# Performance work log

Hardware: AMD Instinct MI355X
Metric: run time of the kernel (lower is better)

Reference implementation:

```python
import jax, jax.numpy as jnp
import numpy as np

N_NODES = 100000
N_EDGES = 1600000
D_IN, D_H, D_OUT = 256, 128, 128


def setup_inputs() -> dict:
    key = jax.random.key(0)
    ks = jax.random.split(key, 8)
    x = jax.random.normal(ks[0], (N_NODES, D_IN), dtype=jnp.float32)
    edge_index = jax.random.randint(ks[1], (2, N_EDGES), 0, N_NODES, dtype=jnp.int64)
    def glorot(k, fan_in, fan_out):
        s = jnp.sqrt(6.0 / (fan_in + fan_out))
        return jax.random.uniform(k, (fan_in, fan_out), jnp.float32, -s, s)
    W1 = glorot(ks[2], D_IN, D_H)
    b1 = jnp.zeros((D_H,), jnp.float32)
    W2 = glorot(ks[3], D_H, D_H)
    b2 = jnp.zeros((D_H,), jnp.float32)
    W3 = glorot(ks[4], D_H, D_OUT)
    b3 = jnp.zeros((D_OUT,), jnp.float32)
    return {"x": x, "edge_index": edge_index,
            "W1": W1, "b1": b1, "W2": W2, "b2": b2, "W3": W3, "b3": b3}


def _gcn_norm(edge_index, n_nodes):
    # PyG GCNConv: add self-loops, symmetric normalization D^-1/2 (A+I) D^-1/2
    loop = jnp.arange(n_nodes, dtype=edge_index.dtype)
    src = jnp.concatenate([edge_index[0], loop])  # source j
    dst = jnp.concatenate([edge_index[1], loop])  # target i
    deg = jax.ops.segment_sum(jnp.ones_like(dst, dtype=jnp.float32), dst,
                              num_segments=n_nodes)
    dinv = jnp.where(deg > 0, jax.lax.rsqrt(deg), 0.0)
    norm = dinv[src] * dinv[dst]  # [E+N]
    return src, dst, norm


def _gcn_conv(h, W, b, src, dst, norm, n_nodes):
    h = h @ W                                   # [N, d_out] transform first
    msg = h[src] * norm[:, None]                # gather + edge-weight
    out = jax.ops.segment_sum(msg, dst, num_segments=n_nodes)  # scatter-add
    return out + b


def reference(x, edge_index, W1, b1, W2, b2, W3, b3):
    n = x.shape[0]
    src, dst, norm = _gcn_norm(edge_index, n)
    h = jax.nn.relu(_gcn_conv(x, W1, b1, src, dst, norm, n))
    h = jax.nn.relu(_gcn_conv(h, W2, b2, src, dst, norm, n))
    return _gcn_conv(h, W3, b3, src, dst, norm, n)
```

## Files before the change

### kernel.cpp

```cpp
#include <hip/hip_runtime.h>
#include <hip/hip_fp16.h>
#include <math.h>


#define N_NODES 100000
#define N_EDGES 1600000

typedef _Float16 f16x8 __attribute__((ext_vector_type(8)));
typedef float    f32x4 __attribute__((ext_vector_type(4)));


__global__ __launch_bounds__(256) void k_zero_int(int* __restrict__ p, int n) {
    int i = blockIdx.x * 256 + threadIdx.x;
    if (i < n) p[i] = 0;
}

__global__ __launch_bounds__(256) void k_count(const int* __restrict__ dst, int* __restrict__ cnt, int E) {
    int e = blockIdx.x * 256 + threadIdx.x;
    if (e < E) atomicAdd(&cnt[dst[e]], 1);
}

__global__ __launch_bounds__(256) void k_scan_block(const int* __restrict__ cnt, int* __restrict__ excl,
                                                    int* __restrict__ bsum, int n) {
    __shared__ int s[256];
    int i = blockIdx.x * 256 + threadIdx.x;
    int v = (i < n) ? ((cnt[i] + 7) & ~7) : 0;
    s[threadIdx.x] = v;
    __syncthreads();
    #pragma unroll
    for (int off = 1; off < 256; off <<= 1) {
        int t = (threadIdx.x >= (unsigned)off) ? s[threadIdx.x - off] : 0;
        __syncthreads();
        s[threadIdx.x] += t;
        __syncthreads();
    }
    if (i < n) excl[i] = s[threadIdx.x] - v;
    if (threadIdx.x == 255) bsum[blockIdx.x] = s[255];
}

__global__ __launch_bounds__(512) void k_scan_partials(int* __restrict__ bsum, int nb) {
    __shared__ int s[512];
    int tid = threadIdx.x;
    int v = (tid < nb) ? bsum[tid] : 0;
    s[tid] = v;
    __syncthreads();
    #pragma unroll
    for (int off = 1; off < 512; off <<= 1) {
        int t = (tid >= (unsigned)off) ? s[tid - off] : 0;
        __syncthreads();
        s[tid] += t;
        __syncthreads();
    }
    if (tid < nb) bsum[tid] = s[tid] - v;
}

__global__ __launch_bounds__(256) void k_finalize(const int* __restrict__ excl, const int* __restrict__ bsum,
                                                  const int* __restrict__ cnt, int* __restrict__ rowptr,
                                                  int* __restrict__ fill, float* __restrict__ dinv, int n) {
    int i = blockIdx.x * 256 + threadIdx.x;
    if (i < n) {
        int rp = excl[i] + bsum[i >> 8];
        rowptr[i] = rp;
        fill[i]   = rp;
        dinv[i]   = rsqrtf((float)(cnt[i] + 1));
    }
}

__global__ __launch_bounds__(256) void k_init_csr(int* __restrict__ csr, int n, unsigned int* __restrict__ phz) {
    int i = blockIdx.x * 256 + threadIdx.x;
    if (i < n) csr[i] = N_NODES;
    if (blockIdx.x == 0 && threadIdx.x < 64) phz[threadIdx.x] = 0;
}

__global__ __launch_bounds__(256) void k_fill_edges(const int* __restrict__ src, const int* __restrict__ dst,
                                                    int* __restrict__ fill, int* __restrict__ csr,
                                                    int E, int lo, int hi) {
    int e = blockIdx.x * 256 + threadIdx.x;
    if (e < E) {
        int d = dst[e];
        if (d >= lo && d < hi) {
            int p = atomicAdd(&fill[d], 1);
            csr[p] = src[e];
        }
    }
}

__global__ __launch_bounds__(256) void k_wpack(const float* __restrict__ W, _Float16* __restrict__ Wpk, int K) {
    int j = blockIdx.x * 256 + threadIdx.x;
    if (j < K * 128) {
        int i  = j & 7;
        int l  = (j >> 3) & 63;
        int tc = (j >> 9) & 7;
        int c  = j >> 12;
        int col = tc * 16 + (l & 15);
        int k   = c * 32 + (l >> 4) * 8 + i;
        float w = W[(size_t)k * 128 + col];
        _Float16 h = (_Float16)w;
        Wpk[j] = h;
        Wpk[(size_t)K * 128 + j] = (_Float16)(w - (float)h);
    }
}


template <int K>
__global__ __launch_bounds__(256) void k_gemm_mfma(const float* __restrict__ X,
                                                   const _Float16* __restrict__ Wpk,
                                                   const float* __restrict__ dinv,
                                                   _Float16* __restrict__ Y, int n) {
    constexpr int NC = K / 32;
    __shared__ float sX[64 * 32];
    const int t    = threadIdx.x;
    const int wave = t >> 6;
    const int lane = t & 63;
    const int lrow = lane & 15;
    const int kgrp = lane >> 4;
    const int row0 = blockIdx.x * 64;
    const int R    = wave * 16 + lrow;
    const _Float16* __restrict__ Wlo = Wpk + (size_t)K * 128;

    const int rs0 = t >> 3,        gs = t & 7;
    const int rs1 = (t >> 3) + 32;
    const int gc0 = (gs ^ (rs0 & 7)) << 2;
    const int gc1 = (gs ^ (rs1 & 7)) << 2;
    const int gr0 = row0 + rs0, gr1 = row0 + rs1;
    const bool ok0 = gr0 < n, ok1 = gr1 < n;
    const float* __restrict__ xr0 = X + (size_t)gr0 * K;
    const float* __restrict__ xr1 = X + (size_t)gr1 * K;

    f32x4 acc[8];
    #pragma unroll
    for (int i = 0; i < 8; ++i) acc[i] = (f32x4){0.f, 0.f, 0.f, 0.f};

    const float4 z4 = make_float4(0.f, 0.f, 0.f, 0.f);
    float4 rv0 = ok0 ? *(const float4*)&xr0[gc0] : z4;
    float4 rv1 = ok1 ? *(const float4*)&xr1[gc1] : z4;
    *(float4*)&sX[(rs0 * 8 + gs) * 4] = rv0;
    *(float4*)&sX[(rs1 * 8 + gs) * 4] = rv1;
    __syncthreads();

    #pragma unroll
    for (int c = 0; c < NC; ++c) {
        if (c + 1 < NC) {
            rv0 = ok0 ? *(const float4*)&xr0[(c + 1) * 32 + gc0] : z4;
            rv1 = ok1 ? *(const float4*)&xr1[(c + 1) * 32 + gc1] : z4;
        }
        float4 x0 = *(const float4*)&sX[(R * 8 + ((kgrp * 2)     ^ (R & 7))) * 4];
        float4 x1 = *(const float4*)&sX[(R * 8 + ((kgrp * 2 + 1) ^ (R & 7))) * 4];
        float xs[8] = {x0.x, x0.y, x0.z, x0.w, x1.x, x1.y, x1.z, x1.w};
        f16x8 ah, al;
        #pragma unroll
        for (int i = 0; i < 8; ++i) {
            _Float16 h = (_Float16)xs[i];
            ah[i] = h;
            al[i] = (_Float16)(xs[i] - (float)h);
        }
        const size_t wb = ((size_t)(c * 8) * 64 + lane) * 8;
        #pragma unroll
        for (int tc = 0; tc < 8; ++tc) {
            f16x8 bh = *(const f16x8*)(Wpk + wb + (size_t)tc * 512);
            f16x8 bl = *(const f16x8*)(Wlo + wb + (size_t)tc * 512);
            acc[tc] = __builtin_amdgcn_mfma_f32_16x16x32_f16(ah, bh, acc[tc], 0, 0, 0);
            acc[tc] = __builtin_amdgcn_mfma_f32_16x16x32_f16(al, bh, acc[tc], 0, 0, 0);
            acc[tc] = __builtin_amdgcn_mfma_f32_16x16x32_f16(ah, bl, acc[tc], 0, 0, 0);
        }
        if (c + 1 < NC) {
            __syncthreads();
            *(float4*)&sX[(rs0 * 8 + gs) * 4] = rv0;
            *(float4*)&sX[(rs1 * 8 + gs) * 4] = rv1;
            __syncthreads();
        }
    }

    #pragma unroll
    for (int r = 0; r < 4; ++r) {
        int grow = row0 + wave * 16 + kgrp * 4 + r;
        if (grow < n) {
            float dv = dinv[grow];
            _Float16* yr = Y + (size_t)grow * 128 + lrow;
            #pragma unroll
            for (int tc = 0; tc < 8; ++tc) yr[tc * 16] = (_Float16)(dv * acc[tc][r]);
        }
    }
}


__device__ __forceinline__ void acc8(float a[8], uint4 u) {
    float2 p;
    p = __half22float2(*(__half2*)&u.x); a[0] += p.x; a[1] += p.y;
    p = __half22float2(*(__half2*)&u.y); a[2] += p.x; a[3] += p.y;
    p = __half22float2(*(__half2*)&u.z); a[4] += p.x; a[5] += p.y;
    p = __half22float2(*(__half2*)&u.w); a[6] += p.x; a[7] += p.y;
}

template <bool RELU>
__global__ __launch_bounds__(256) void k_agg(const __half* __restrict__ H, const int* __restrict__ rowptr,
                                             const int* __restrict__ cnt, const int* __restrict__ csr,
                                             const float* __restrict__ dinv, const float* __restrict__ bias,
                                             float* __restrict__ out, int n) {
    const int lane  = threadIdx.x & 63;
    const int q     = lane >> 4;
    const int fl    = lane & 15;
    const int wave0 = (int)((blockIdx.x * 256 + threadIdx.x) >> 6);
    const int nwave = (int)((gridDim.x * 256) >> 6);
    const uint4* __restrict__ Hu = (const uint4*)H;
    const float4 b0 = *(const float4*)&bias[fl * 8];
    const float4 b1 = *(const float4*)&bias[fl * 8 + 4];

    const int nquad = n >> 2;
    for (int g = wave0; g < nquad; g += nwave) {
        const int node = g * 4 + q;
        float a[8];
        {
            uint4 u = Hu[(size_t)node * 16 + fl];
            float2 p;
            p = __half22float2(*(__half2*)&u.x); a[0] = p.x; a[1] = p.y;
            p = __half22float2(*(__half2*)&u.y); a[2] = p.x; a[3] = p.y;
            p = __half22float2(*(__half2*)&u.z); a[4] = p.x; a[5] = p.y;
            p = __half22float2(*(__half2*)&u.w); a[6] = p.x; a[7] = p.y;
        }

        const int c0 = rowptr[node];
        const int cn = cnt[node];
        for (int e8 = 0; e8 < cn; e8 += 8) {
            const int4* qp = (const int4*)(csr + c0 + e8);
            int4 qa = qp[0], qb = qp[1];
            uint4 u0 = Hu[(size_t)qa.x * 16 + fl];
            uint4 u1 = Hu[(size_t)qa.y * 16 + fl];
            uint4 u2 = Hu[(size_t)qa.z * 16 + fl];
            uint4 u3 = Hu[(size_t)qa.w * 16 + fl];
            uint4 u4 = Hu[(size_t)qb.x * 16 + fl];
            uint4 u5 = Hu[(size_t)qb.y * 16 + fl];
            uint4 u6 = Hu[(size_t)qb.z * 16 + fl];
            uint4 u7 = Hu[(size_t)qb.w * 16 + fl];
            acc8(a, u0); acc8(a, u1); acc8(a, u2); acc8(a, u3);
            acc8(a, u4); acc8(a, u5); acc8(a, u6); acc8(a, u7);
        }

        const float dv = dinv[node];
        float4 o0, o1;
        o0.x = fmaf(dv, a[0], b0.x); o0.y = fmaf(dv, a[1], b0.y);
        o0.z = fmaf(dv, a[2], b0.z); o0.w = fmaf(dv, a[3], b0.w);
        o1.x = fmaf(dv, a[4], b1.x); o1.y = fmaf(dv, a[5], b1.y);
        o1.z = fmaf(dv, a[6], b1.z); o1.w = fmaf(dv, a[7], b1.w);
        if (RELU) {
            o0.x = fmaxf(o0.x, 0.f); o0.y = fmaxf(o0.y, 0.f);
            o0.z = fmaxf(o0.z, 0.f); o0.w = fmaxf(o0.w, 0.f);
            o1.x = fmaxf(o1.x, 0.f); o1.y = fmaxf(o1.y, 0.f);
            o1.z = fmaxf(o1.z, 0.f); o1.w = fmaxf(o1.w, 0.f);
        }
        *(float4*)&out[(size_t)node * 128 + fl * 8]     = o0;
        *(float4*)&out[(size_t)node * 128 + fl * 8 + 4] = o1;
    }
}


extern "C" void kernel_launch(void* const* d_in, const int* in_sizes, int n_in,
                              void* d_out, int out_size, void* d_ws, size_t ws_size,
                              hipStream_t stream) {
    const float* x  = (const float*)d_in[0];
    const int*   ei = (const int*)d_in[1];
    const float* W1 = (const float*)d_in[2];
    const float* b1 = (const float*)d_in[3];
    const float* W2 = (const float*)d_in[4];
    const float* b2 = (const float*)d_in[5];
    const float* W3 = (const float*)d_in[6];
    const float* b3 = (const float*)d_in[7];
    float* out = (float*)d_out;

    const int N = N_NODES, E = N_EDGES;
    const int EP = E + 7 * N + 64;
    const int* src = ei;
    const int* dst = ei + E;

    char* w = (char*)d_ws;
    auto alloc = [&](size_t bytes) -> void* {
        void* p = (void*)w;
        w += (bytes + 255) & ~(size_t)255;
        return p;
    };
    int*      cnt    = (int*)alloc((size_t)N * 4);
    int*      excl   = (int*)alloc((size_t)N * 4);
    int*      bsum   = (int*)alloc(4096);
    int*      rowptr = (int*)alloc((size_t)N * 4);
    int*      fill   = (int*)alloc((size_t)N * 4);
    float*    dinv   = (float*)alloc((size_t)N * 4);
    int*      csr    = (int*)alloc((size_t)EP * 4);
    _Float16* Ph     = (_Float16*)alloc((size_t)(N + 8) * 128 * 2);
    _Float16* Wpk    = (_Float16*)alloc((size_t)2 * 256 * 128 * 2);
    float*    Q      = out;

    const int nbN = (N + 255) / 256;
    const int nbE = (E + 255) / 256;
    const int nbP = (EP + 255) / 256;

    k_zero_int<<<nbN, 256, 0, stream>>>(cnt, N);
    k_count<<<nbE, 256, 0, stream>>>(dst, cnt, E);
    k_scan_block<<<nbN, 256, 0, stream>>>(cnt, excl, bsum, N);
    k_scan_partials<<<1, 512, 0, stream>>>(bsum, nbN);
    k_finalize<<<nbN, 256, 0, stream>>>(excl, bsum, cnt, rowptr, fill, dinv, N);
    k_init_csr<<<nbP, 256, 0, stream>>>(csr, EP, (unsigned int*)(Ph + (size_t)N * 128));
    for (int r = 0; r < 4; ++r) {
        int lo = r * (N / 4);
        int hi = (r == 3) ? N : (r + 1) * (N / 4);
        k_fill_edges<<<nbE, 256, 0, stream>>>(src, dst, fill, csr, E, lo, hi);
    }

    const int gemm_grid = (N + 63) / 64;
    const int agg_grid  = 2048;

    k_wpack<<<(256 * 128 + 255) / 256, 256, 0, stream>>>(W1, Wpk, 256);
    k_gemm_mfma<256><<<gemm_grid, 256, 0, stream>>>(x, Wpk, dinv, Ph, N);
    k_agg<true><<<agg_grid, 256, 0, stream>>>((const __half*)Ph, rowptr, cnt, csr, dinv, b1, Q, N);
    k_wpack<<<(128 * 128 + 255) / 256, 256, 0, stream>>>(W2, Wpk, 128);
    k_gemm_mfma<128><<<gemm_grid, 256, 0, stream>>>(Q, Wpk, dinv, Ph, N);
    k_agg<true><<<agg_grid, 256, 0, stream>>>((const __half*)Ph, rowptr, cnt, csr, dinv, b2, Q, N);
    k_wpack<<<(128 * 128 + 255) / 256, 256, 0, stream>>>(W3, Wpk, 128);
    k_gemm_mfma<128><<<gemm_grid, 256, 0, stream>>>(Q, Wpk, dinv, Ph, N);
    k_agg<false><<<agg_grid, 256, 0, stream>>>((const __half*)Ph, rowptr, cnt, csr, dinv, b3, out, N);
}
```

Baseline: 464.3 us.

## Double GEMM row tile per block and split each node's edges across wave quarters

The MFMA GEMM now handles 128 rows per block: each wave computes two 16-row tiles, so every W fragment load is reused twice, at the cost of more accumulator registers. The aggregation kernel now gives each node a whole wave instead of a 16-lane quarter. The four quarters each gather two neighbours per 8-edge chunk and are combined with cross-lane shuffles. This is meant to even out load imbalance from varying degrees and shorten the per-node dependency chain, but it adds shuffle work and leaves three quarters of the lanes idle during the output write.

```diff
diff --git a/kernel.cpp b/kernel.cpp
--- a/kernel.cpp
+++ b/kernel.cpp
@@ -108,34 +108,48 @@
                                                    const float* __restrict__ dinv,
                                                    _Float16* __restrict__ Y, int n) {
     constexpr int NC = K / 32;
-    __shared__ float sX[64 * 32];
+    __shared__ float sX[128 * 32];
     const int t    = threadIdx.x;
     const int wave = t >> 6;
     const int lane = t & 63;
     const int lrow = lane & 15;
     const int kgrp = lane >> 4;
-    const int row0 = blockIdx.x * 64;
-    const int R    = wave * 16 + lrow;
+    const int row0 = blockIdx.x * 128;
+    const int R0   = wave * 32 + lrow;
+    const int R1   = R0 + 16;
     const _Float16* __restrict__ Wlo = Wpk + (size_t)K * 128;
 
-    const int rs0 = t >> 3,        gs = t & 7;
-    const int rs1 = (t >> 3) + 32;
-    const int gc0 = (gs ^ (rs0 & 7)) << 2;
-    const int gc1 = (gs ^ (rs1 & 7)) << 2;
-    const int gr0 = row0 + rs0, gr1 = row0 + rs1;
-    const bool ok0 = gr0 < n, ok1 = gr1 < n;
-    const float* __restrict__ xr0 = X + (size_t)gr0 * K;
-    const float* __restrict__ xr1 = X + (size_t)gr1 * K;
-
-    f32x4 acc[8];
-    #pragma unroll
-    for (int i = 0; i < 8; ++i) acc[i] = (f32x4){0.f, 0.f, 0.f, 0.f};
+    const int gs  = t & 7;
+    const int rsb = t >> 3;
+    const float* __restrict__ xr0 = X + (size_t)(row0 + rsb)      * K;
+    const float* __restrict__ xr1 = X + (size_t)(row0 + rsb + 32) * K;
+    const float* __restrict__ xr2 = X + (size_t)(row0 + rsb + 64) * K;
+    const float* __restrict__ xr3 = X + (size_t)(row0 + rsb + 96) * K;
+    const bool ok0 = row0 + rsb      < n;
+    const bool ok1 = row0 + rsb + 32 < n;
+    const bool ok2 = row0 + rsb + 64 < n;
+    const bool ok3 = row0 + rsb + 96 < n;
+    const int gc0 = (gs ^ ( rsb       & 7)) << 2;
+    const int gc1 = (gs ^ ((rsb + 32) & 7)) << 2;
+    const int gc2 = (gs ^ ((rsb + 64) & 7)) << 2;
+    const int gc3 = (gs ^ ((rsb + 96) & 7)) << 2;
+
+    f32x4 acc0[8], acc1[8];
+    #pragma unroll
+    for (int i = 0; i < 8; ++i) {
+        acc0[i] = (f32x4){0.f, 0.f, 0.f, 0.f};
+        acc1[i] = (f32x4){0.f, 0.f, 0.f, 0.f};
+    }
 
     const float4 z4 = make_float4(0.f, 0.f, 0.f, 0.f);
     float4 rv0 = ok0 ? *(const float4*)&xr0[gc0] : z4;
     float4 rv1 = ok1 ? *(const float4*)&xr1[gc1] : z4;
-    *(float4*)&sX[(rs0 * 8 + gs) * 4] = rv0;
-    *(float4*)&sX[(rs1 * 8 + gs) * 4] = rv1;
+    float4 rv2 = ok2 ? *(const float4*)&xr2[gc2] : z4;
+    float4 rv3 = ok3 ? *(const float4*)&xr3[gc3] : z4;
+    *(float4*)&sX[((rsb     ) * 8 + gs) * 4] = rv0;
+    *(float4*)&sX[((rsb + 32) * 8 + gs) * 4] = rv1;
+    *(float4*)&sX[((rsb + 64) * 8 + gs) * 4] = rv2;
+    *(float4*)&sX[((rsb + 96) * 8 + gs) * 4] = rv3;
     __syncthreads();
 
     #pragma unroll
@@ -143,42 +157,65 @@
         if (c + 1 < NC) {
             rv0 = ok0 ? *(const float4*)&xr0[(c + 1) * 32 + gc0] : z4;
             rv1 = ok1 ? *(const float4*)&xr1[(c + 1) * 32 + gc1] : z4;
-        }
-        float4 x0 = *(const float4*)&sX[(R * 8 + ((kgrp * 2)     ^ (R & 7))) * 4];
-        float4 x1 = *(const float4*)&sX[(R * 8 + ((kgrp * 2 + 1) ^ (R & 7))) * 4];
-        float xs[8] = {x0.x, x0.y, x0.z, x0.w, x1.x, x1.y, x1.z, x1.w};
-        f16x8 ah, al;
+            rv2 = ok2 ? *(const float4*)&xr2[(c + 1) * 32 + gc2] : z4;
+            rv3 = ok3 ? *(const float4*)&xr3[(c + 1) * 32 + gc3] : z4;
+        }
+        float4 x0a = *(const float4*)&sX[(R0 * 8 + ((kgrp * 2)     ^ (R0 & 7))) * 4];
+        float4 x0b = *(const float4*)&sX[(R0 * 8 + ((kgrp * 2 + 1) ^ (R0 & 7))) * 4];
+        float4 x1a = *(const float4*)&sX[(R1 * 8 + ((kgrp * 2)     ^ (R1 & 7))) * 4];
+        float4 x1b = *(const float4*)&sX[(R1 * 8 + ((kgrp * 2 + 1) ^ (R1 & 7))) * 4];
+        float xs0[8] = {x0a.x, x0a.y, x0a.z, x0a.w, x0b.x, x0b.y, x0b.z, x0b.w};
+        float xs1[8] = {x1a.x, x1a.y, x1a.z, x1a.w, x1b.x, x1b.y, x1b.z, x1b.w};
+        f16x8 ah0, al0, ah1, al1;
         #pragma unroll
         for (int i = 0; i < 8; ++i) {
-            _Float16 h = (_Float16)xs[i];
-            ah[i] = h;
-            al[i] = (_Float16)(xs[i] - (float)h);
+            _Float16 h0 = (_Float16)xs0[i];
+            ah0[i] = h0;
+            al0[i] = (_Float16)(xs0[i] - (float)h0);
+            _Float16 h1 = (_Float16)xs1[i];
+            ah1[i] = h1;
+            al1[i] = (_Float16)(xs1[i] - (float)h1);
         }
         const size_t wb = ((size_t)(c * 8) * 64 + lane) * 8;
         #pragma unroll
         for (int tc = 0; tc < 8; ++tc) {
             f16x8 bh = *(const f16x8*)(Wpk + wb + (size_t)tc * 512);
             f16x8 bl = *(const f16x8*)(Wlo + wb + (size_t)tc * 512);
-            acc[tc] = __builtin_amdgcn_mfma_f32_16x16x32_f16(ah, bh, acc[tc], 0, 0, 0);
-            acc[tc] = __builtin_amdgcn_mfma_f32_16x16x32_f16(al, bh, acc[tc], 0, 0, 0);
-            acc[tc] = __builtin_amdgcn_mfma_f32_16x16x32_f16(ah, bl, acc[tc], 0, 0, 0);
+            acc0[tc] = __builtin_amdgcn_mfma_f32_16x16x32_f16(ah0, bh, acc0[tc], 0, 0, 0);
+            acc0[tc] = __builtin_amdgcn_mfma_f32_16x16x32_f16(al0, bh, acc0[tc], 0, 0, 0);
+            acc0[tc] = __builtin_amdgcn_mfma_f32_16x16x32_f16(ah0, bl, acc0[tc], 0, 0, 0);
+            acc1[tc] = __builtin_amdgcn_mfma_f32_16x16x32_f16(ah1, bh, acc1[tc], 0, 0, 0);
+            acc1[tc] = __builtin_amdgcn_mfma_f32_16x16x32_f16(al1, bh, acc1[tc], 0, 0, 0);
+            acc1[tc] = __builtin_amdgcn_mfma_f32_16x16x32_f16(ah1, bl, acc1[tc], 0, 0, 0);
         }
         if (c + 1 < NC) {
             __syncthreads();
-            *(float4*)&sX[(rs0 * 8 + gs) * 4] = rv0;
-            *(float4*)&sX[(rs1 * 8 + gs) * 4] = rv1;
+            *(float4*)&sX[((rsb     ) * 8 + gs) * 4] = rv0;
+            *(float4*)&sX[((rsb + 32) * 8 + gs) * 4] = rv1;
+            *(float4*)&sX[((rsb + 64) * 8 + gs) * 4] = rv2;
+            *(float4*)&sX[((rsb + 96) * 8 + gs) * 4] = rv3;
             __syncthreads();
         }
     }
 
     #pragma unroll
     for (int r = 0; r < 4; ++r) {
-        int grow = row0 + wave * 16 + kgrp * 4 + r;
+        int grow = row0 + wave * 32 + kgrp * 4 + r;
         if (grow < n) {
             float dv = dinv[grow];
             _Float16* yr = Y + (size_t)grow * 128 + lrow;
             #pragma unroll
-            for (int tc = 0; tc < 8; ++tc) yr[tc * 16] = (_Float16)(dv * acc[tc][r]);
+            for (int tc = 0; tc < 8; ++tc) yr[tc * 16] = (_Float16)(dv * acc0[tc][r]);
+        }
+    }
+    #pragma unroll
+    for (int r = 0; r < 4; ++r) {
+        int grow = row0 + wave * 32 + 16 + kgrp * 4 + r;
+        if (grow < n) {
+            float dv = dinv[grow];
+            _Float16* yr = Y + (size_t)grow * 128 + lrow;
+            #pragma unroll
+            for (int tc = 0; tc < 8; ++tc) yr[tc * 16] = (_Float16)(dv * acc1[tc][r]);
         }
     }
 }
@@ -203,14 +240,10 @@
     const int wave0 = (int)((blockIdx.x * 256 + threadIdx.x) >> 6);
     const int nwave = (int)((gridDim.x * 256) >> 6);
     const uint4* __restrict__ Hu = (const uint4*)H;
-    const float4 b0 = *(const float4*)&bias[fl * 8];
-    const float4 b1 = *(const float4*)&bias[fl * 8 + 4];
-
-    const int nquad = n >> 2;
-    for (int g = wave0; g < nquad; g += nwave) {
-        const int node = g * 4 + q;
-        float a[8];
-        {
+
+    for (int node = wave0; node < n; node += nwave) {
+        float a[8] = {0.f, 0.f, 0.f, 0.f, 0.f, 0.f, 0.f, 0.f};
+        if (q == 0) {
             uint4 u = Hu[(size_t)node * 16 + fl];
             float2 p;
             p = __half22float2(*(__half2*)&u.x); a[0] = p.x; a[1] = p.y;
@@ -221,35 +254,39 @@
 
         const int c0 = rowptr[node];
         const int cn = cnt[node];
-        for (int e8 = 0; e8 < cn; e8 += 8) {
-            const int4* qp = (const int4*)(csr + c0 + e8);
-            int4 qa = qp[0], qb = qp[1];
-            uint4 u0 = Hu[(size_t)qa.x * 16 + fl];
-            uint4 u1 = Hu[(size_t)qa.y * 16 + fl];
-            uint4 u2 = Hu[(size_t)qa.z * 16 + fl];
-            uint4 u3 = Hu[(size_t)qa.w * 16 + fl];
-            uint4 u4 = Hu[(size_t)qb.x * 16 + fl];
-            uint4 u5 = Hu[(size_t)qb.y * 16 + fl];
-            uint4 u6 = Hu[(size_t)qb.z * 16 + fl];
-            uint4 u7 = Hu[(size_t)qb.w * 16 + fl];
-            acc8(a, u0); acc8(a, u1); acc8(a, u2); acc8(a, u3);
-            acc8(a, u4); acc8(a, u5); acc8(a, u6); acc8(a, u7);
-        }
-
-        const float dv = dinv[node];
-        float4 o0, o1;
-        o0.x = fmaf(dv, a[0], b0.x); o0.y = fmaf(dv, a[1], b0.y);
-        o0.z = fmaf(dv, a[2], b0.z); o0.w = fmaf(dv, a[3], b0.w);
-        o1.x = fmaf(dv, a[4], b1.x); o1.y = fmaf(dv, a[5], b1.y);
-        o1.z = fmaf(dv, a[6], b1.z); o1.w = fmaf(dv, a[7], b1.w);
-        if (RELU) {
-            o0.x = fmaxf(o0.x, 0.f); o0.y = fmaxf(o0.y, 0.f);
-            o0.z = fmaxf(o0.z, 0.f); o0.w = fmaxf(o0.w, 0.f);
-            o1.x = fmaxf(o1.x, 0.f); o1.y = fmaxf(o1.y, 0.f);
-            o1.z = fmaxf(o1.z, 0.f); o1.w = fmaxf(o1.w, 0.f);
-        }
-        *(float4*)&out[(size_t)node * 128 + fl * 8]     = o0;
-        *(float4*)&out[(size_t)node * 128 + fl * 8 + 4] = o1;
+        #pragma unroll 2
+        for (int e = 0; e < cn; e += 8) {
+            int2 id = *(const int2*)&csr[c0 + e + 2 * q];
+            uint4 u0 = Hu[(size_t)id.x * 16 + fl];
+            uint4 u1 = Hu[(size_t)id.y * 16 + fl];
+            acc8(a, u0);
+            acc8(a, u1);
+        }
+
+        #pragma unroll
+        for (int i = 0; i < 8; ++i) {
+            a[i] += __shfl_xor(a[i], 16);
+            a[i] += __shfl_xor(a[i], 32);
+        }
+
+        if (q == 0) {
+            const float dv = dinv[node];
+            const float4 b0 = *(const float4*)&bias[fl * 8];
+            const float4 b1 = *(const float4*)&bias[fl * 8 + 4];
+            float4 o0, o1;
+            o0.x = fmaf(dv, a[0], b0.x); o0.y = fmaf(dv, a[1], b0.y);
+            o0.z = fmaf(dv, a[2], b0.z); o0.w = fmaf(dv, a[3], b0.w);
+            o1.x = fmaf(dv, a[4], b1.x); o1.y = fmaf(dv, a[5], b1.y);
+            o1.z = fmaf(dv, a[6], b1.z); o1.w = fmaf(dv, a[7], b1.w);
+            if (RELU) {
+                o0.x = fmaxf(o0.x, 0.f); o0.y = fmaxf(o0.y, 0.f);
+                o0.z = fmaxf(o0.z, 0.f); o0.w = fmaxf(o0.w, 0.f);
+                o1.x = fmaxf(o1.x, 0.f); o1.y = fmaxf(o1.y, 0.f);
+                o1.z = fmaxf(o1.z, 0.f); o1.w = fmaxf(o1.w, 0.f);
+            }
+            *(float4*)&out[(size_t)node * 128 + fl * 8]     = o0;
+            *(float4*)&out[(size_t)node * 128 + fl * 8 + 4] = o1;
+        }
     }
 }
 
@@ -305,7 +342,7 @@
         k_fill_edges<<<nbE, 256, 0, stream>>>(src, dst, fill, csr, E, lo, hi);
     }
 
-    const int gemm_grid = (N + 63) / 64;
+    const int gemm_grid = (N + 127) / 128;
     const int agg_grid  = 2048;
 
     k_wpack<<<(256 * 128 + 255) / 256, 256, 0, stream>>>(W1, Wpk, 256);
```

Result: slower. 478.4 us (+3.0%).

## Hold W fragments in registers and split output columns across waves in MFMA GEMM

Applied to the files above, without the earlier changes.

Each wave now owns 32 output columns across all 64 rows and loads its W hi/lo fragments into registers once, instead of re-reading W from global memory for every K chunk. X is converted to the fp16 hi/lo split once per element during staging and stored in double-buffered shared memory, so the conversion is no longer repeated by every wave, and one barrier per chunk is removed. The cost is many more registers for preloaded W (NC*4 f16x8 vectors), which for K=256 may lower occupancy.

```diff
diff --git a/kernel.cpp b/kernel.cpp
--- a/kernel.cpp
+++ b/kernel.cpp
@@ -108,77 +108,100 @@
                                                    const float* __restrict__ dinv,
                                                    _Float16* __restrict__ Y, int n) {
     constexpr int NC = K / 32;
-    __shared__ float sX[64 * 32];
+    __shared__ __align__(16) _Float16 sAh[2][4][64][8];
+    __shared__ __align__(16) _Float16 sAl[2][4][64][8];
     const int t    = threadIdx.x;
     const int wave = t >> 6;
     const int lane = t & 63;
     const int lrow = lane & 15;
     const int kgrp = lane >> 4;
     const int row0 = blockIdx.x * 64;
-    const int R    = wave * 16 + lrow;
     const _Float16* __restrict__ Wlo = Wpk + (size_t)K * 128;
 
-    const int rs0 = t >> 3,        gs = t & 7;
-    const int rs1 = (t >> 3) + 32;
-    const int gc0 = (gs ^ (rs0 & 7)) << 2;
-    const int gc1 = (gs ^ (rs1 & 7)) << 2;
-    const int gr0 = row0 + rs0, gr1 = row0 + rs1;
-    const bool ok0 = gr0 < n, ok1 = gr1 < n;
-    const float* __restrict__ xr0 = X + (size_t)gr0 * K;
-    const float* __restrict__ xr1 = X + (size_t)gr1 * K;
-
-    f32x4 acc[8];
-    #pragma unroll
-    for (int i = 0; i < 8; ++i) acc[i] = (f32x4){0.f, 0.f, 0.f, 0.f};
+    f16x8 bh[NC][2], bl[NC][2];
+    #pragma unroll
+    for (int c = 0; c < NC; ++c)
+        #pragma unroll
+        for (int j = 0; j < 2; ++j) {
+            const size_t idx = ((size_t)(c * 8 + wave * 2 + j) * 64 + lane) * 8;
+            bh[c][j] = *(const f16x8*)(Wpk + idx);
+            bl[c][j] = *(const f16x8*)(Wlo + idx);
+        }
+
+    const int srow = t >> 2;
+    const int skg  = t & 3;
+    const int sfrag = srow >> 4;
+    const int slane = (skg << 4) | (srow & 15);
+    const bool sok = row0 + srow < n;
+    const float* __restrict__ xrow = X + (size_t)(row0 + srow) * K + skg * 8;
+
+    f32x4 acc[4][2];
+    #pragma unroll
+    for (int f = 0; f < 4; ++f)
+        #pragma unroll
+        for (int j = 0; j < 2; ++j) acc[f][j] = (f32x4){0.f, 0.f, 0.f, 0.f};
 
     const float4 z4 = make_float4(0.f, 0.f, 0.f, 0.f);
-    float4 rv0 = ok0 ? *(const float4*)&xr0[gc0] : z4;
-    float4 rv1 = ok1 ? *(const float4*)&xr1[gc1] : z4;
-    *(float4*)&sX[(rs0 * 8 + gs) * 4] = rv0;
-    *(float4*)&sX[(rs1 * 8 + gs) * 4] = rv1;
-    __syncthreads();
-
-    #pragma unroll
-    for (int c = 0; c < NC; ++c) {
-        if (c + 1 < NC) {
-            rv0 = ok0 ? *(const float4*)&xr0[(c + 1) * 32 + gc0] : z4;
-            rv1 = ok1 ? *(const float4*)&xr1[(c + 1) * 32 + gc1] : z4;
-        }
-        float4 x0 = *(const float4*)&sX[(R * 8 + ((kgrp * 2)     ^ (R & 7))) * 4];
-        float4 x1 = *(const float4*)&sX[(R * 8 + ((kgrp * 2 + 1) ^ (R & 7))) * 4];
-        float xs[8] = {x0.x, x0.y, x0.z, x0.w, x1.x, x1.y, x1.z, x1.w};
-        f16x8 ah, al;
+    float4 ra = sok ? *(const float4*)&xrow[0] : z4;
+    float4 rb = sok ? *(const float4*)&xrow[4] : z4;
+    {
+        float xs[8] = {ra.x, ra.y, ra.z, ra.w, rb.x, rb.y, rb.z, rb.w};
+        f16x8 hi, lo;
         #pragma unroll
         for (int i = 0; i < 8; ++i) {
             _Float16 h = (_Float16)xs[i];
-            ah[i] = h;
-            al[i] = (_Float16)(xs[i] - (float)h);
-        }
-        const size_t wb = ((size_t)(c * 8) * 64 + lane) * 8;
-        #pragma unroll
-        for (int tc = 0; tc < 8; ++tc) {
-            f16x8 bh = *(const f16x8*)(Wpk + wb + (size_t)tc * 512);
-            f16x8 bl = *(const f16x8*)(Wlo + wb + (size_t)tc * 512);
-            acc[tc] = __builtin_amdgcn_mfma_f32_16x16x32_f16(ah, bh, acc[tc], 0, 0, 0);
-            acc[tc] = __builtin_amdgcn_mfma_f32_16x16x32_f16(al, bh, acc[tc], 0, 0, 0);
-            acc[tc] = __builtin_amdgcn_mfma_f32_16x16x32_f16(ah, bl, acc[tc], 0, 0, 0);
-        }
+            hi[i] = h;
+            lo[i] = (_Float16)(xs[i] - (float)h);
+        }
+        *(f16x8*)&sAh[0][sfrag][slane][0] = hi;
+        *(f16x8*)&sAl[0][sfrag][slane][0] = lo;
+    }
+    __syncthreads();
+
+    #pragma unroll
+    for (int c = 0; c < NC; ++c) {
+        const int cur = c & 1;
         if (c + 1 < NC) {
+            ra = sok ? *(const float4*)&xrow[(c + 1) * 32] : z4;
+            rb = sok ? *(const float4*)&xrow[(c + 1) * 32 + 4] : z4;
+        }
+        #pragma unroll
+        for (int f = 0; f < 4; ++f) {
+            f16x8 ah = *(const f16x8*)&sAh[cur][f][lane][0];
+            f16x8 al = *(const f16x8*)&sAl[cur][f][lane][0];
+            #pragma unroll
+            for (int j = 0; j < 2; ++j) {
+                acc[f][j] = __builtin_amdgcn_mfma_f32_16x16x32_f16(ah, bh[c][j], acc[f][j], 0, 0, 0);
+                acc[f][j] = __builtin_amdgcn_mfma_f32_16x16x32_f16(al, bh[c][j], acc[f][j], 0, 0, 0);
+                acc[f][j] = __builtin_amdgcn_mfma_f32_16x16x32_f16(ah, bl[c][j], acc[f][j], 0, 0, 0);
+            }
+        }
+        if (c + 1 < NC) {
+            float xs[8] = {ra.x, ra.y, ra.z, ra.w, rb.x, rb.y, rb.z, rb.w};
+            f16x8 hi, lo;
+            #pragma unroll
+            for (int i = 0; i < 8; ++i) {
+                _Float16 h = (_Float16)xs[i];
+                hi[i] = h;
+                lo[i] = (_Float16)(xs[i] - (float)h);
+            }
+            *(f16x8*)&sAh[cur ^ 1][sfrag][slane][0] = hi;
+            *(f16x8*)&sAl[cur ^ 1][sfrag][slane][0] = lo;
             __syncthreads();
-            *(float4*)&sX[(rs0 * 8 + gs) * 4] = rv0;
-            *(float4*)&sX[(rs1 * 8 + gs) * 4] = rv1;
-            __syncthreads();
-        }
-    }
-
-    #pragma unroll
-    for (int r = 0; r < 4; ++r) {
-        int grow = row0 + wave * 16 + kgrp * 4 + r;
-        if (grow < n) {
-            float dv = dinv[grow];
-            _Float16* yr = Y + (size_t)grow * 128 + lrow;
-            #pragma unroll
-            for (int tc = 0; tc < 8; ++tc) yr[tc * 16] = (_Float16)(dv * acc[tc][r]);
+        }
+    }
+
+    #pragma unroll
+    for (int f = 0; f < 4; ++f) {
+        #pragma unroll
+        for (int r = 0; r < 4; ++r) {
+            int grow = row0 + f * 16 + kgrp * 4 + r;
+            if (grow < n) {
+                float dv = dinv[grow];
+                _Float16* yr = Y + (size_t)grow * 128 + wave * 32 + lrow;
+                yr[0]  = (_Float16)(dv * acc[f][0][r]);
+                yr[16] = (_Float16)(dv * acc[f][1][r]);
+            }
         }
     }
 }
```

After: 533.8 us. +15.0%, slower.

## Stage 128-wide K slabs in padded LDS for GEMM; split degree count into four node ranges

Applied to the files above, without the earlier changes.

The GEMM now loads 128 columns of X per stage into a padded LDS tile (stride 33 float4) instead of 32 columns per stage with an XOR swizzle. This cuts the number of barrier/refill rounds to one or two per block, at the cost of more LDS per block, which may lower occupancy. The degree-count kernel is also split into four launches, each handling only destination nodes in one quarter of the node range. This narrows the atomic footprint per pass, the same approach the existing fill_edges step already uses, but it reads the edge list four times.

```diff
diff --git a/kernel.cpp b/kernel.cpp
--- a/kernel.cpp
+++ b/kernel.cpp
@@ -15,9 +15,13 @@
     if (i < n) p[i] = 0;
 }
 
-__global__ __launch_bounds__(256) void k_count(const int* __restrict__ dst, int* __restrict__ cnt, int E) {
+__global__ __launch_bounds__(256) void k_count(const int* __restrict__ dst, int* __restrict__ cnt,
+                                               int E, int lo, int hi) {
     int e = blockIdx.x * 256 + threadIdx.x;
-    if (e < E) atomicAdd(&cnt[dst[e]], 1);
+    if (e < E) {
+        int d = dst[e];
+        if (d >= lo && d < hi) atomicAdd(&cnt[d], 1);
+    }
 }
 
 __global__ __launch_bounds__(256) void k_scan_block(const int* __restrict__ cnt, int* __restrict__ excl,
@@ -107,8 +111,8 @@
                                                    const _Float16* __restrict__ Wpk,
                                                    const float* __restrict__ dinv,
                                                    _Float16* __restrict__ Y, int n) {
-    constexpr int NC = K / 32;
-    __shared__ float sX[64 * 32];
+    constexpr int NS = K / 128;
+    __shared__ float sX[64 * 33 * 4];
     const int t    = threadIdx.x;
     const int wave = t >> 6;
     const int lane = t & 63;
@@ -118,55 +122,63 @@
     const int R    = wave * 16 + lrow;
     const _Float16* __restrict__ Wlo = Wpk + (size_t)K * 128;
 
-    const int rs0 = t >> 3,        gs = t & 7;
-    const int rs1 = (t >> 3) + 32;
-    const int gc0 = (gs ^ (rs0 & 7)) << 2;
-    const int gc1 = (gs ^ (rs1 & 7)) << 2;
-    const int gr0 = row0 + rs0, gr1 = row0 + rs1;
-    const bool ok0 = gr0 < n, ok1 = gr1 < n;
-    const float* __restrict__ xr0 = X + (size_t)gr0 * K;
-    const float* __restrict__ xr1 = X + (size_t)gr1 * K;
+    const int sr = t >> 5;
+    const int sg = t & 31;
 
     f32x4 acc[8];
     #pragma unroll
     for (int i = 0; i < 8; ++i) acc[i] = (f32x4){0.f, 0.f, 0.f, 0.f};
 
     const float4 z4 = make_float4(0.f, 0.f, 0.f, 0.f);
-    float4 rv0 = ok0 ? *(const float4*)&xr0[gc0] : z4;
-    float4 rv1 = ok1 ? *(const float4*)&xr1[gc1] : z4;
-    *(float4*)&sX[(rs0 * 8 + gs) * 4] = rv0;
-    *(float4*)&sX[(rs1 * 8 + gs) * 4] = rv1;
+
+    #pragma unroll
+    for (int i = 0; i < 8; ++i) {
+        int r  = sr + i * 8;
+        int gr = row0 + r;
+        float4 v = (gr < n) ? *(const float4*)&X[(size_t)gr * K + sg * 4] : z4;
+        *(float4*)&sX[(r * 33 + sg) * 4] = v;
+    }
     __syncthreads();
 
     #pragma unroll
-    for (int c = 0; c < NC; ++c) {
-        if (c + 1 < NC) {
-            rv0 = ok0 ? *(const float4*)&xr0[(c + 1) * 32 + gc0] : z4;
-            rv1 = ok1 ? *(const float4*)&xr1[(c + 1) * 32 + gc1] : z4;
-        }
-        float4 x0 = *(const float4*)&sX[(R * 8 + ((kgrp * 2)     ^ (R & 7))) * 4];
-        float4 x1 = *(const float4*)&sX[(R * 8 + ((kgrp * 2 + 1) ^ (R & 7))) * 4];
-        float xs[8] = {x0.x, x0.y, x0.z, x0.w, x1.x, x1.y, x1.z, x1.w};
-        f16x8 ah, al;
+    for (int s = 0; s < NS; ++s) {
+        float4 rv[8];
+        if (s + 1 < NS) {
+            #pragma unroll
+            for (int i = 0; i < 8; ++i) {
+                int r  = sr + i * 8;
+                int gr = row0 + r;
+                rv[i] = (gr < n) ? *(const float4*)&X[(size_t)gr * K + (s + 1) * 128 + sg * 4] : z4;
+            }
+        }
         #pragma unroll
-        for (int i = 0; i < 8; ++i) {
-            _Float16 h = (_Float16)xs[i];
-            ah[i] = h;
-            al[i] = (_Float16)(xs[i] - (float)h);
-        }
-        const size_t wb = ((size_t)(c * 8) * 64 + lane) * 8;
-        #pragma unroll
-        for (int tc = 0; tc < 8; ++tc) {
-            f16x8 bh = *(const f16x8*)(Wpk + wb + (size_t)tc * 512);
-            f16x8 bl = *(const f16x8*)(Wlo + wb + (size_t)tc * 512);
-            acc[tc] = __builtin_amdgcn_mfma_f32_16x16x32_f16(ah, bh, acc[tc], 0, 0, 0);
-            acc[tc] = __builtin_amdgcn_mfma_f32_16x16x32_f16(al, bh, acc[tc], 0, 0, 0);
-            acc[tc] = __builtin_amdgcn_mfma_f32_16x16x32_f16(ah, bl, acc[tc], 0, 0, 0);
-        }
-        if (c + 1 < NC) {
+        for (int cc = 0; cc < 4; ++cc) {
+            const int c = s * 4 + cc;
+            float4 x0 = *(const float4*)&sX[(R * 33 + cc * 8 + kgrp * 2)     * 4];
+            float4 x1 = *(const float4*)&sX[(R * 33 + cc * 8 + kgrp * 2 + 1) * 4];
+            float xs[8] = {x0.x, x0.y, x0.z, x0.w, x1.x, x1.y, x1.z, x1.w};
+            f16x8 ah, al;
+            #pragma unroll
+            for (int i = 0; i < 8; ++i) {
+                _Float16 h = (_Float16)xs[i];
+                ah[i] = h;
+                al[i] = (_Float16)(xs[i] - (float)h);
+            }
+            const size_t wb = ((size_t)(c * 8) * 64 + lane) * 8;
+            #pragma unroll
+            for (int tc = 0; tc < 8; ++tc) {
+                f16x8 bh = *(const f16x8*)(Wpk + wb + (size_t)tc * 512);
+                f16x8 bl = *(const f16x8*)(Wlo + wb + (size_t)tc * 512);
+                acc[tc] = __builtin_amdgcn_mfma_f32_16x16x32_f16(ah, bh, acc[tc], 0, 0, 0);
+                acc[tc] = __builtin_amdgcn_mfma_f32_16x16x32_f16(al, bh, acc[tc], 0, 0, 0);
+                acc[tc] = __builtin_amdgcn_mfma_f32_16x16x32_f16(ah, bl, acc[tc], 0, 0, 0);
+            }
+        }
+        if (s + 1 < NS) {
             __syncthreads();
-            *(float4*)&sX[(rs0 * 8 + gs) * 4] = rv0;
-            *(float4*)&sX[(rs1 * 8 + gs) * 4] = rv1;
+            #pragma unroll
+            for (int i = 0; i < 8; ++i)
+                *(float4*)&sX[((sr + i * 8) * 33 + sg) * 4] = rv[i];
             __syncthreads();
         }
     }
@@ -294,7 +306,11 @@
     const int nbP = (EP + 255) / 256;
 
     k_zero_int<<<nbN, 256, 0, stream>>>(cnt, N);
-    k_count<<<nbE, 256, 0, stream>>>(dst, cnt, E);
+    for (int r = 0; r < 4; ++r) {
+        int lo = r * (N / 4);
+        int hi = (r == 3) ? N : (r + 1) * (N / 4);
+        k_count<<<nbE, 256, 0, stream>>>(dst, cnt, E, lo, hi);
+    }
     k_scan_block<<<nbN, 256, 0, stream>>>(cnt, excl, bsum, N);
     k_scan_partials<<<1, 512, 0, stream>>>(bsum, nbN);
     k_finalize<<<nbN, 256, 0, stream>>>(excl, bsum, cnt, rowptr, fill, dinv, N);
```

Measured after the change: 521.3 us. +12.3%, slower.
